# Kernel optimization log

Hardware: AMD Instinct MI355X
Metric: run time of the kernel (lower is better)

Reference implementation:

```python
import jax, jax.numpy as jnp
import numpy as np

H = 50  # hidden_size
B = 4096
T = 256


def setup_inputs() -> dict:
    key = jax.random.key(0)
    ks = jax.random.split(key, 9)
    s = 1.0 / np.sqrt(H).astype(np.float32)  # matches torch U(-1/sqrt(H),1/sqrt(H)) scale
    x = jax.random.normal(ks[0], (B, T, 1), jnp.float32)
    w_ih0 = jax.random.normal(ks[1], (4 * H, 1), jnp.float32) * s
    w_hh0 = jax.random.normal(ks[2], (4 * H, H), jnp.float32) * s
    b0 = jax.random.normal(ks[3], (4 * H,), jnp.float32) * s
    w_ih = jax.random.normal(ks[4], (4, 4 * H, H), jnp.float32) * s
    w_hh = jax.random.normal(ks[5], (4, 4 * H, H), jnp.float32) * s
    b = jax.random.normal(ks[6], (4, 4 * H), jnp.float32) * s
    fc_w = jax.random.normal(ks[7], (1, H), jnp.float32) * s
    fc_b = jax.random.normal(ks[8], (1,), jnp.float32) * s
    return dict(x=x, w_ih0=w_ih0, w_hh0=w_hh0, b0=b0,
                w_ih=w_ih, w_hh=w_hh, b=b, fc_w=fc_w, fc_b=fc_b)


def _lstm_layer(x_tbd, w_ih, w_hh, bias):
    # x_tbd: [T, B, D_in]; w_ih: [4H, D_in]; w_hh: [4H, H]; bias: [4H]
    # Precompute input-side gate preactivations for all timesteps (one big GEMM).
    xg = jnp.einsum('tbi,gi->tbg', x_tbd, w_ih) + bias  # [T, B, 4H]
    Bsz = x_tbd.shape[1]
    h0 = jnp.zeros((Bsz, H), x_tbd.dtype)
    c0 = jnp.zeros((Bsz, H), x_tbd.dtype)

    def step(carry, xg_t):
        h, c = carry
        g = xg_t + h @ w_hh.T                  # [B, 4H]
        i, f, gc, o = jnp.split(g, 4, axis=-1)  # torch gate order: i, f, g, o
        c = jax.nn.sigmoid(f) * c + jax.nn.sigmoid(i) * jnp.tanh(gc)
        h = jax.nn.sigmoid(o) * jnp.tanh(c)
        return (h, c), h

    (hT, _), ys = jax.lax.scan(step, (h0, c0), xg)
    return ys, hT  # ys: [T, B, H], hT: [B, H]


def reference(x, w_ih0, w_hh0, b0, w_ih, w_hh, b, fc_w, fc_b):
    # x: [B, T, 1] (batch_first) -> time-major for scan
    xt = jnp.transpose(x, (1, 0, 2))  # [T, B, 1]
    ys, hT = _lstm_layer(xt, w_ih0, w_hh0, b0)
    for l in range(4):  # 4 more stacked layers (num_layers=5)
        ys, hT = _lstm_layer(ys, w_ih[l], w_hh[l], b[l])
    # dropout is identity in eval mode; fc on final hidden of top layer
    return hT @ fc_w.T + fc_b  # [B, 1]
```

## Files before the change

kernel.cpp:

```cpp
#include <hip/hip_runtime.h>
#include <cstdint>
#include <cstddef>


#define HSZ   50
#define G4    200
#define TS    256
#define RPB   4
#define NB    (4096 / RPB)
#define NT    256
#define XH    112
#define HOFF  56

__device__ __forceinline__ float sigf(float x) {
  return __builtin_amdgcn_rcpf(1.0f + __expf(-x));
}
__device__ __forceinline__ float tanh_f(float x) {
  return fmaf(2.0f, __builtin_amdgcn_rcpf(1.0f + __expf(-2.0f * x)), -1.0f);
}

__device__ __forceinline__ void load_row50(const float* __restrict__ p, float4 w[13]) {
  #pragma unroll
  for (int kk = 0; kk < 12; ++kk) {
    float2 e0 = *(const float2*)(p + kk * 4);
    float2 e1 = *(const float2*)(p + kk * 4 + 2);
    w[kk] = make_float4(e0.x, e0.y, e1.x, e1.y);
  }
  float2 tl = *(const float2*)(p + 48);
  w[12] = make_float4(tl.x, tl.y, 0.0f, 0.0f);
}

__global__ void __launch_bounds__(NT, 2)
lstm5_kernel(const float* __restrict__ x,
             const float* __restrict__ w_ih0, const float* __restrict__ w_hh0,
             const float* __restrict__ b0,
             const float* __restrict__ w_ih,  const float* __restrict__ w_hh,
             const float* __restrict__ b,
             const float* __restrict__ fc_w,  const float* __restrict__ fc_b,
             float* __restrict__ out, float* __restrict__ ys)
{
  __shared__ __align__(16) float s_xh[RPB * XH];
  __shared__ __align__(16) float s_g[G4 * RPB];

  const int tid  = threadIdx.x;
  const int blk  = blockIdx.x;
  const int row0 = blk * RPB;
  const bool gt  = (tid < G4);
  const int  g   = gt ? tid : (G4 - 1);
  const int  pr  = tid & 3;
  const int  phu = tid >> 2;
  float* __restrict__ ysb = ys + (size_t)blk * (TS * G4);

  float4 wih[13], whh[13];
  float  bias = 0.0f, wx0 = 0.0f;

  for (int layer = 0; layer < 5; ++layer) {
    if (layer == 0) {
      wx0  = w_ih0[g];
      load_row50(w_hh0 + (size_t)g * HSZ, whh);
      bias = b0[g];
    } else {
      const float* Wih = w_ih + (size_t)(layer - 1) * G4 * HSZ;
      const float* Whh = w_hh + (size_t)(layer - 1) * G4 * HSZ;
      load_row50(Wih + (size_t)g * HSZ, wih);
      load_row50(Whh + (size_t)g * HSZ, whh);
      bias = b[(size_t)(layer - 1) * G4 + g];
    }

    for (int i = tid; i < RPB * XH; i += NT) s_xh[i] = 0.0f;
    __syncthreads();
    if (layer == 0) {
      if (tid < RPB) s_xh[tid * XH] = x[(size_t)(row0 + tid) * TS];
    } else if (gt) {
      s_xh[pr * XH + phu] = ysb[tid];
    }
    float cst = 0.0f;
    __syncthreads();

    for (int t = 0; t < TS; ++t) {
      const int nt2 = (t + 1 < TS) ? (t + 1) : t;
      float pf = 0.0f;
      if (layer == 0) {
        if (tid < RPB) pf = x[(size_t)(row0 + tid) * TS + nt2];
      } else if (gt) {
        pf = ysb[nt2 * G4 + tid];
      }

      float a[RPB];
      #pragma unroll
      for (int r = 0; r < RPB; ++r) a[r] = bias;

      #pragma unroll
      for (int r = 0; r < RPB; ++r) {
        const float* bx = s_xh + r * XH;
        if (layer == 0) {
          a[r] = fmaf(wx0, bx[0], a[r]);
        } else {
          #pragma unroll
          for (int kk = 0; kk < 13; ++kk) {
            float4 xv = *(const float4*)(bx + kk * 4);
            a[r] = fmaf(wih[kk].x, xv.x, a[r]);
            a[r] = fmaf(wih[kk].y, xv.y, a[r]);
            a[r] = fmaf(wih[kk].z, xv.z, a[r]);
            a[r] = fmaf(wih[kk].w, xv.w, a[r]);
          }
        }
        #pragma unroll
        for (int kk = 0; kk < 13; ++kk) {
          float4 hv = *(const float4*)(bx + HOFF + kk * 4);
          a[r] = fmaf(whh[kk].x, hv.x, a[r]);
          a[r] = fmaf(whh[kk].y, hv.y, a[r]);
          a[r] = fmaf(whh[kk].z, hv.z, a[r]);
          a[r] = fmaf(whh[kk].w, hv.w, a[r]);
        }
      }
      if (gt) *(float4*)&s_g[g * 4] = make_float4(a[0], a[1], a[2], a[3]);
      __syncthreads();

      if (layer == 0) {
        if (tid < RPB) s_xh[tid * XH] = pf;
      } else if (gt) {
        s_xh[pr * XH + phu] = pf;
      }

      if (gt) {
        float gi = s_g[ phu        * 4 + pr];
        float gf = s_g[(phu +  50) * 4 + pr];
        float gg = s_g[(phu + 100) * 4 + pr];
        float go = s_g[(phu + 150) * 4 + pr];
        float c  = fmaf(sigf(gf), cst, sigf(gi) * tanh_f(gg));
        cst = c;
        float h  = sigf(go) * tanh_f(c);
        s_xh[pr * XH + HOFF + phu] = h;
        if (layer < 4) ysb[t * G4 + tid] = h;
      }
      __syncthreads();
    }
  }

  if (tid < RPB) {
    float a2 = fc_b[0];
    const float* hr = s_xh + tid * XH + HOFF;
    #pragma unroll
    for (int k = 0; k < HSZ; ++k) a2 = fmaf(hr[k], fc_w[k], a2);
    out[row0 + tid] = a2;
  }
}

extern "C" void kernel_launch(void* const* d_in, const int* in_sizes, int n_in,
                              void* d_out, int out_size, void* d_ws, size_t ws_size,
                              hipStream_t stream) {
  (void)in_sizes; (void)n_in; (void)out_size; (void)ws_size;
  const float* x     = (const float*)d_in[0];
  const float* w_ih0 = (const float*)d_in[1];
  const float* w_hh0 = (const float*)d_in[2];
  const float* b0    = (const float*)d_in[3];
  const float* w_ih  = (const float*)d_in[4];
  const float* w_hh  = (const float*)d_in[5];
  const float* b     = (const float*)d_in[6];
  const float* fc_w  = (const float*)d_in[7];
  const float* fc_b  = (const float*)d_in[8];
  float* out = (float*)d_out;
  float* ys  = (float*)d_ws;

  hipLaunchKernelGGL(lstm5_kernel, dim3(NB), dim3(NT), 0, stream,
                     x, w_ih0, w_hh0, b0, w_ih, w_hh, b, fc_w, fc_b, out, ys);
}
```

Before: 10.74 ms.

## Broadcast hidden state via readlane and double rows per block

Each block now handles 8 batch rows instead of 4. Each lane loads one hidden or input element per row into a register, and the matvec broadcasts it with `__builtin_amdgcn_readlane` instead of reading float4 vectors from shared memory. Weights are kept as scalar arrays of 50, and the ys layout changes to [t][row][h]. The goal is to cut LDS traffic, halve the block count, and reuse each weight register across more rows. The cost is more accumulators and register pressure, and readlane with a constant index becomes a scalar move that may serialise.

Measured after the change: 10.27 ms. -4.3%, faster.

```diff
diff --git a/kernel.cpp b/kernel.cpp
--- a/kernel.cpp
+++ b/kernel.cpp
@@ -6,11 +6,11 @@
 #define HSZ   50
 #define G4    200
 #define TS    256
-#define RPB   4
+#define RPB   8
 #define NB    (4096 / RPB)
 #define NT    256
-#define XH    112
-#define HOFF  56
+#define HP    64
+#define YROW  (RPB * HSZ)
 
 __device__ __forceinline__ float sigf(float x) {
   return __builtin_amdgcn_rcpf(1.0f + __expf(-x));
@@ -18,16 +18,16 @@
 __device__ __forceinline__ float tanh_f(float x) {
   return fmaf(2.0f, __builtin_amdgcn_rcpf(1.0f + __expf(-2.0f * x)), -1.0f);
 }
+__device__ __forceinline__ float rdlane(float v, int k) {
+  return __int_as_float(__builtin_amdgcn_readlane(__float_as_int(v), k));
+}
 
-__device__ __forceinline__ void load_row50(const float* __restrict__ p, float4 w[13]) {
+__device__ __forceinline__ void load50(const float* __restrict__ p, float w[HSZ]) {
   #pragma unroll
-  for (int kk = 0; kk < 12; ++kk) {
-    float2 e0 = *(const float2*)(p + kk * 4);
-    float2 e1 = *(const float2*)(p + kk * 4 + 2);
-    w[kk] = make_float4(e0.x, e0.y, e1.x, e1.y);
+  for (int q = 0; q < 25; ++q) {
+    float2 e = *(const float2*)(p + q * 2);
+    w[q * 2] = e.x;  w[q * 2 + 1] = e.y;
   }
-  float2 tl = *(const float2*)(p + 48);
-  w[12] = make_float4(tl.x, tl.y, 0.0f, 0.0f);
 }
 
 __global__ void __launch_bounds__(NT, 2)
@@ -39,108 +39,118 @@
              const float* __restrict__ fc_w,  const float* __restrict__ fc_b,
              float* __restrict__ out, float* __restrict__ ys)
 {
-  __shared__ __align__(16) float s_xh[RPB * XH];
-  __shared__ __align__(16) float s_g[G4 * RPB];
+  __shared__ __align__(16) float s_h[RPB * HP];
+  __shared__ __align__(16) float s_g[RPB * G4];
 
   const int tid  = threadIdx.x;
   const int blk  = blockIdx.x;
   const int row0 = blk * RPB;
+  const int lane = tid & 63;
+  const int lcl  = (lane < HSZ) ? lane : (HSZ - 1);
   const bool gt  = (tid < G4);
   const int  g   = gt ? tid : (G4 - 1);
-  const int  pr  = tid & 3;
-  const int  phu = tid >> 2;
-  float* __restrict__ ysb = ys + (size_t)blk * (TS * G4);
+  const int  phu = tid & 63;
+  const int  pr0 = tid >> 6;
+  const bool pw  = (phu < HSZ);
+  float* __restrict__ ysb = ys + (size_t)blk * (TS * YROW);
 
-  float4 wih[13], whh[13];
-  float  bias = 0.0f, wx0 = 0.0f;
+  float wI[HSZ], wH[HSZ];
+  float bias = 0.0f, wx0 = 0.0f;
 
   for (int layer = 0; layer < 5; ++layer) {
     if (layer == 0) {
       wx0  = w_ih0[g];
-      load_row50(w_hh0 + (size_t)g * HSZ, whh);
+      load50(w_hh0 + (size_t)g * HSZ, wH);
       bias = b0[g];
     } else {
-      const float* Wih = w_ih + (size_t)(layer - 1) * G4 * HSZ;
-      const float* Whh = w_hh + (size_t)(layer - 1) * G4 * HSZ;
-      load_row50(Wih + (size_t)g * HSZ, wih);
-      load_row50(Whh + (size_t)g * HSZ, whh);
+      load50(w_ih + (size_t)(layer - 1) * G4 * HSZ + (size_t)g * HSZ, wI);
+      load50(w_hh + (size_t)(layer - 1) * G4 * HSZ + (size_t)g * HSZ, wH);
       bias = b[(size_t)(layer - 1) * G4 + g];
     }
-
-    for (int i = tid; i < RPB * XH; i += NT) s_xh[i] = 0.0f;
-    __syncthreads();
+    s_h[tid] = 0.0f;  s_h[tid + NT] = 0.0f;
+    float cst0 = 0.0f, cst1 = 0.0f;
+    float vx[RPB];
     if (layer == 0) {
-      if (tid < RPB) s_xh[tid * XH] = x[(size_t)(row0 + tid) * TS];
-    } else if (gt) {
-      s_xh[pr * XH + phu] = ysb[tid];
+      #pragma unroll
+      for (int r = 0; r < RPB; ++r) vx[r] = x[(size_t)(row0 + r) * TS];
+    } else {
+      #pragma unroll
+      for (int r = 0; r < RPB; ++r) vx[r] = ysb[r * HSZ + lcl];
     }
-    float cst = 0.0f;
     __syncthreads();
 
     for (int t = 0; t < TS; ++t) {
+      float vh[RPB];
+      #pragma unroll
+      for (int r = 0; r < RPB; ++r) vh[r] = s_h[r * HP + lcl];
+
       const int nt2 = (t + 1 < TS) ? (t + 1) : t;
-      float pf = 0.0f;
+      float vxn[RPB];
       if (layer == 0) {
-        if (tid < RPB) pf = x[(size_t)(row0 + tid) * TS + nt2];
-      } else if (gt) {
-        pf = ysb[nt2 * G4 + tid];
+        #pragma unroll
+        for (int r = 0; r < RPB; ++r) vxn[r] = x[(size_t)(row0 + r) * TS + nt2];
+      } else {
+        #pragma unroll
+        for (int r = 0; r < RPB; ++r) vxn[r] = ysb[nt2 * YROW + r * HSZ + lcl];
       }
 
       float a[RPB];
       #pragma unroll
       for (int r = 0; r < RPB; ++r) a[r] = bias;
 
-      #pragma unroll
-      for (int r = 0; r < RPB; ++r) {
-        const float* bx = s_xh + r * XH;
-        if (layer == 0) {
-          a[r] = fmaf(wx0, bx[0], a[r]);
-        } else {
+      if (layer == 0) {
+        #pragma unroll
+        for (int r = 0; r < RPB; ++r) a[r] = fmaf(wx0, vx[r], a[r]);
+      } else {
+        #pragma unroll
+        for (int k = 0; k < HSZ; ++k) {
           #pragma unroll
-          for (int kk = 0; kk < 13; ++kk) {
-            float4 xv = *(const float4*)(bx + kk * 4);
-            a[r] = fmaf(wih[kk].x, xv.x, a[r]);
-            a[r] = fmaf(wih[kk].y, xv.y, a[r]);
-            a[r] = fmaf(wih[kk].z, xv.z, a[r]);
-            a[r] = fmaf(wih[kk].w, xv.w, a[r]);
-          }
-        }
-        #pragma unroll
-        for (int kk = 0; kk < 13; ++kk) {
-          float4 hv = *(const float4*)(bx + HOFF + kk * 4);
-          a[r] = fmaf(whh[kk].x, hv.x, a[r]);
-          a[r] = fmaf(whh[kk].y, hv.y, a[r]);
-          a[r] = fmaf(whh[kk].z, hv.z, a[r]);
-          a[r] = fmaf(whh[kk].w, hv.w, a[r]);
+          for (int r = 0; r < RPB; ++r)
+            a[r] = fmaf(wI[k], rdlane(vx[r], k), a[r]);
         }
       }
-      if (gt) *(float4*)&s_g[g * 4] = make_float4(a[0], a[1], a[2], a[3]);
-      __syncthreads();
-
-      if (layer == 0) {
-        if (tid < RPB) s_xh[tid * XH] = pf;
-      } else if (gt) {
-        s_xh[pr * XH + phu] = pf;
+      #pragma unroll
+      for (int k = 0; k < HSZ; ++k) {
+        #pragma unroll
+        for (int r = 0; r < RPB; ++r)
+          a[r] = fmaf(wH[k], rdlane(vh[r], k), a[r]);
       }
 
       if (gt) {
-        float gi = s_g[ phu        * 4 + pr];
-        float gf = s_g[(phu +  50) * 4 + pr];
-        float gg = s_g[(phu + 100) * 4 + pr];
-        float go = s_g[(phu + 150) * 4 + pr];
-        float c  = fmaf(sigf(gf), cst, sigf(gi) * tanh_f(gg));
-        cst = c;
-        float h  = sigf(go) * tanh_f(c);
-        s_xh[pr * XH + HOFF + phu] = h;
-        if (layer < 4) ysb[t * G4 + tid] = h;
+        #pragma unroll
+        for (int r = 0; r < RPB; ++r) s_g[r * G4 + g] = a[r];
       }
       __syncthreads();
+
+      if (pw) {
+        {
+          const float* gp = s_g + pr0 * G4 + phu;
+          float c = fmaf(sigf(gp[50]), cst0, sigf(gp[0]) * tanh_f(gp[100]));
+          cst0 = c;
+          float h = sigf(gp[150]) * tanh_f(c);
+          s_h[pr0 * HP + phu] = h;
+          if (layer < 4) ysb[t * YROW + pr0 * HSZ + phu] = h;
+        }
+        {
+          const int pr1 = pr0 + 4;
+          const float* gp = s_g + pr1 * G4 + phu;
+          float c = fmaf(sigf(gp[50]), cst1, sigf(gp[0]) * tanh_f(gp[100]));
+          cst1 = c;
+          float h = sigf(gp[150]) * tanh_f(c);
+          s_h[pr1 * HP + phu] = h;
+          if (layer < 4) ysb[t * YROW + pr1 * HSZ + phu] = h;
+        }
+      }
+      __syncthreads();
+
+      #pragma unroll
+      for (int r = 0; r < RPB; ++r) vx[r] = vxn[r];
     }
   }
 
   if (tid < RPB) {
     float a2 = fc_b[0];
-    const float* hr = s_xh + tid * XH + HOFF;
+    const float* hr = s_h + tid * HP;
     #pragma unroll
     for (int k = 0; k < HSZ; ++k) a2 = fmaf(hr[k], fc_w[k], a2);
     out[row0 + tid] = a2;
```
